# Optimization experiments

Hardware: AMD Instinct MI355X
Metric: run time of the kernel (lower is better)

The kernel has to match this reference:

```python
import jax, jax.numpy as jnp
import numpy as np

N_NODES = 100000
N_EDGES = 3200000
IN_DIM = 256


def gcn_conv(x, src, dst, W, b):
    # PyG GCNConv: add self-loops, symmetric normalization D^-1/2 A D^-1/2
    n = x.shape[0]
    loop = jnp.arange(n)
    s = jnp.concatenate([src, loop])
    d = jnp.concatenate([dst, loop])
    deg = jax.ops.segment_sum(jnp.ones(d.shape, x.dtype), d, num_segments=n)
    dinv = jnp.where(deg > 0, jax.lax.rsqrt(deg), 0.0).astype(x.dtype)
    norm = dinv[s] * dinv[d]                      # [E+N]
    h = x @ W                                     # [N, out] transform first (out < in)
    msg = h[s] * norm[:, None]                    # gather + scale
    out = jax.ops.segment_sum(msg, d, num_segments=n)  # scatter-add
    return out + b


def setup_inputs() -> dict:
    key = jax.random.key(0)
    ks = jax.random.split(key, 8)
    x = jax.random.normal(ks[0], (N_NODES, IN_DIM), dtype=jnp.float32)
    edge_index = jax.random.randint(ks[1], (2, N_EDGES), 0, N_NODES, dtype=jnp.int64)
    # Glorot-ish scaled params
    W1 = jax.random.normal(ks[2], (IN_DIM, 64), dtype=jnp.float32) / np.sqrt(IN_DIM)
    b1 = jnp.zeros((64,), jnp.float32)
    W2 = jax.random.normal(ks[3], (64, 32), dtype=jnp.float32) / np.sqrt(64)
    b2 = jnp.zeros((32,), jnp.float32)
    fc_w = jax.random.normal(ks[4], (1, 32), dtype=jnp.float32) / np.sqrt(32)
    fc_b = jnp.zeros((1,), jnp.float32)
    return {"x": x, "edge_index": edge_index, "W1": W1, "b1": b1,
            "W2": W2, "b2": b2, "fc_w": fc_w, "fc_b": fc_b}


def reference(x, edge_index, W1, b1, W2, b2, fc_w, fc_b):
    src, dst = edge_index[0], edge_index[1]
    h = jax.nn.relu(gcn_conv(x, src, dst, W1, b1))   # [N, 64]
    h = jax.nn.relu(gcn_conv(h, src, dst, W2, b2))   # [N, 32]
    pooled = h.mean(axis=0)                          # [32]
    return pooled @ fc_w.T + fc_b                    # [1]
```

## Files before the change

kernel.cpp:

```cpp
#include <hip/hip_runtime.h>
#include <hip/hip_fp16.h>

#ifndef F1
#define F1 64
#define F2 32
#endif

#define NBLK 512
#define BSH  7
#define BNODES 128

typedef _Float16 half8 __attribute__((ext_vector_type(8)));
typedef float floatx4 __attribute__((ext_vector_type(4)));

__global__ __launch_bounds__(256) void scan_blocks_kernel(const int* __restrict__ in,
                                                          int* __restrict__ tmp,
                                                          int* __restrict__ blk_sums, int n) {
    __shared__ int sdata[256];
    int t = threadIdx.x;
    int base = blockIdx.x * 1024 + t * 4;
    int v[4];
#pragma unroll
    for (int j = 0; j < 4; ++j) v[j] = (base + j < n) ? in[base + j] : 0;
    int mysum = v[0] + v[1] + v[2] + v[3];
    sdata[t] = mysum;
    __syncthreads();
    for (int ofs = 1; ofs < 256; ofs <<= 1) {
        int val = (t >= ofs) ? sdata[t - ofs] : 0;
        __syncthreads();
        sdata[t] += val;
        __syncthreads();
    }
    int incl = sdata[t];
    int excl = incl - mysum;
    if (t == 255) blk_sums[blockIdx.x] = incl;
    int run = excl;
#pragma unroll
    for (int j = 0; j < 4; ++j) {
        if (base + j < n) tmp[base + j] = run;
        run += v[j];
    }
}

__global__ __launch_bounds__(512) void scan_sums_kernel(const int* __restrict__ blk_sums,
                                                        int* __restrict__ blk_scanned, int nb) {
    __shared__ int sdata[512];
    int t = threadIdx.x;
    int mine = (t < nb) ? blk_sums[t] : 0;
    sdata[t] = mine;
    __syncthreads();
    for (int ofs = 1; ofs < 512; ofs <<= 1) {
        int val = (t >= ofs) ? sdata[t - ofs] : 0;
        __syncthreads();
        sdata[t] += val;
        __syncthreads();
    }
    blk_scanned[t] = sdata[t] - mine;
}


__global__ __launch_bounds__(256) void bucket_hist_prep_kernel(const int* __restrict__ dst,
                                                               int* __restrict__ hist_T,
                                                               const float* __restrict__ W1,
                                                               const float* __restrict__ W2,
                                                               __half* __restrict__ W1t,
                                                               __half* __restrict__ W2t,
                                                               float* __restrict__ out,
                                                               int E, int CH, int NB) {
    int b = blockIdx.x;
    if (b == NBLK) {
        if (threadIdx.x == 0) out[0] = 0.f;
        for (int e = threadIdx.x; e < 64 * 256; e += 256) {
            int n = e >> 8, k = e & 255;
            W1t[e] = __float2half(W1[k * 64 + n]);
        }
        for (int e = threadIdx.x; e < 32 * 64; e += 256) {
            int n = e >> 6, k = e & 63;
            W2t[e] = __float2half(W2[k * 32 + n]);
        }
        return;
    }
    __shared__ int lh[1024];
    for (int i = threadIdx.x; i < NB; i += 256) lh[i] = 0;
    __syncthreads();
    int start = b * CH, end = min(E, start + CH);
    for (int e0 = start + threadIdx.x * 4; e0 < end; e0 += 1024) {
        if (e0 + 4 <= end) {
            int4 d4 = *reinterpret_cast<const int4*>(dst + e0);
            atomicAdd(&lh[d4.x >> BSH], 1);
            atomicAdd(&lh[d4.y >> BSH], 1);
            atomicAdd(&lh[d4.z >> BSH], 1);
            atomicAdd(&lh[d4.w >> BSH], 1);
        } else {
            for (int e = e0; e < end; ++e) atomicAdd(&lh[dst[e] >> BSH], 1);
        }
    }
    __syncthreads();
    for (int k = threadIdx.x; k < NB; k += 256)
        hist_T[k * NBLK + b] = lh[k];
}

__global__ __launch_bounds__(256) void bucket_scatter_kernel(const int* __restrict__ src,
                                                             const int* __restrict__ dst,
                                                             const int* __restrict__ tmp,
                                                             const int* __restrict__ bscan,
                                                             int* __restrict__ buck,
                                                             int E, int CH, int NB) {
    __shared__ int cur[1024];
    int b = blockIdx.x;
    for (int i = threadIdx.x; i < NB; i += 256) {
        int idx = i * NBLK + b;
        cur[i] = tmp[idx] + bscan[idx >> 10];
    }
    __syncthreads();
    int start = b * CH, end = min(E, start + CH);
    for (int e0 = start + threadIdx.x * 4; e0 < end; e0 += 1024) {
        if (e0 + 4 <= end) {
            int4 s4 = *reinterpret_cast<const int4*>(src + e0);
            int4 d4 = *reinterpret_cast<const int4*>(dst + e0);
            int p0 = atomicAdd(&cur[d4.x >> BSH], 1);
            buck[p0] = (s4.x << BSH) | (d4.x & (BNODES - 1));
            int p1 = atomicAdd(&cur[d4.y >> BSH], 1);
            buck[p1] = (s4.y << BSH) | (d4.y & (BNODES - 1));
            int p2 = atomicAdd(&cur[d4.z >> BSH], 1);
            buck[p2] = (s4.z << BSH) | (d4.z & (BNODES - 1));
            int p3 = atomicAdd(&cur[d4.w >> BSH], 1);
            buck[p3] = (s4.w << BSH) | (d4.w & (BNODES - 1));
        } else {
            for (int e = e0; e < end; ++e) {
                int d = dst[e];
                int pos = atomicAdd(&cur[d >> BSH], 1);
                buck[pos] = (src[e] << BSH) | (d & (BNODES - 1));
            }
        }
    }
}

__global__ __launch_bounds__(256) void bucket_deg_fill_kernel(const int* __restrict__ buck,
                                                              const int* __restrict__ tmp,
                                                              const int* __restrict__ bscan,
                                                              int* __restrict__ deg,
                                                              float* __restrict__ dinv,
                                                              int* __restrict__ row_off,
                                                              int* __restrict__ csr,
                                                              int E, int N, int NB) {
    __shared__ int cnt[BNODES];
    __shared__ int sc[BNODES];
    __shared__ int lrow[BNODES];
    __shared__ int lcur[BNODES];
    int k = blockIdx.x;
    int tid = threadIdx.x;
    if (tid < BNODES) { cnt[tid] = 0; lcur[tid] = 0; }
    __syncthreads();
    int i0 = k * NBLK;
    int bs = tmp[i0] + bscan[i0 >> 10];
    int be = E;
    if (k + 1 < NB) {
        int i1 = (k + 1) * NBLK;
        be = tmp[i1] + bscan[i1 >> 10];
    }
    for (int e = bs + tid; e < be; e += 256)
        atomicAdd(&cnt[buck[e] & (BNODES - 1)], 1);
    __syncthreads();
    if (tid < BNODES) sc[tid] = cnt[tid];
    __syncthreads();
    for (int ofs = 1; ofs < BNODES; ofs <<= 1) {
        int v = (tid >= ofs && tid < BNODES) ? sc[tid - ofs] : 0;
        __syncthreads();
        if (tid < BNODES) sc[tid] += v;
        __syncthreads();
    }
    if (tid < BNODES) {
        int excl = sc[tid] - cnt[tid];
        lrow[tid] = bs + excl;
        int i = (k << BSH) + tid;
        if (i < N) {
            deg[i] = cnt[tid];
            dinv[i] = rsqrtf((float)(cnt[tid] + 1));
            row_off[i] = bs + excl;
        }
    }
    __syncthreads();
    for (int e = bs + tid; e < be; e += 256) {
        int p = buck[e];
        int li = p & (BNODES - 1);
        int pos = lrow[li] + atomicAdd(&lcur[li], 1);
        csr[pos] = p >> BSH;
    }
}


__device__ __forceinline__ int swz(int p, int r) { return (p ^ ((r >> 1) & 3)) << 4; }

template <bool AF32, int K, int BN>
__global__ __launch_bounds__(256) void gemm_mfma_kernel(const void* __restrict__ Aptr,
                                                        const __half* __restrict__ Bt,
                                                        const float* __restrict__ dinv,
                                                        __half* __restrict__ C,
                                                        int M) {
    constexpr int NT = BN / 16;
    __shared__ half8 Ash[64 * 4];
    __shared__ half8 Bsh[BN * 4];
    char* Ab = (char*)Ash;
    char* Bb = (char*)Bsh;
    int tid = threadIdx.x;
    int w = tid >> 6;
    int l = tid & 63;
    int row0 = blockIdx.x * 64;
    int sr = tid >> 2, sp = tid & 3;
    int fr = l & 15, fp = l >> 4;
    int arow = w * 16 + fr;
    int a_off = arow * 64 + swz(fp, arow);

    floatx4 acc[NT];
#pragma unroll
    for (int c = 0; c < NT; ++c) acc[c] = (floatx4){0.f, 0.f, 0.f, 0.f};

    for (int k0 = 0; k0 < K; k0 += 32) {
        half8 av = {};
        int gr = row0 + sr;
        if (gr < M) {
            if constexpr (AF32) {
                const float* A = (const float*)Aptr;
                float4 f0 = *(const float4*)(A + (size_t)gr * K + k0 + sp * 8);
                float4 f1 = *(const float4*)(A + (size_t)gr * K + k0 + sp * 8 + 4);
                av[0] = (_Float16)f0.x; av[1] = (_Float16)f0.y;
                av[2] = (_Float16)f0.z; av[3] = (_Float16)f0.w;
                av[4] = (_Float16)f1.x; av[5] = (_Float16)f1.y;
                av[6] = (_Float16)f1.z; av[7] = (_Float16)f1.w;
            } else {
                const __half* A = (const __half*)Aptr;
                av = *(const half8*)(A + (size_t)gr * K + k0 + sp * 8);
            }
        }
        *(half8*)(Ab + sr * 64 + swz(sp, sr)) = av;
        if (tid < BN * 4) {
            int n = tid >> 2, p = tid & 3;
            half8 bv = *(const half8*)(Bt + (size_t)n * K + k0 + p * 8);
            *(half8*)(Bb + n * 64 + swz(p, n)) = bv;
        }
        __syncthreads();
        half8 a = *(const half8*)(Ab + a_off);
#pragma unroll
        for (int c = 0; c < NT; ++c) {
            int col = c * 16 + fr;
            half8 b = *(const half8*)(Bb + col * 64 + swz(fp, col));
            acc[c] = __builtin_amdgcn_mfma_f32_16x16x32_f16(a, b, acc[c], 0, 0, 0);
        }
        __syncthreads();
    }
#pragma unroll
    for (int i = 0; i < 4; ++i) {
        int r = row0 + w * 16 + fp * 4 + i;
        if (r < M) {
            float dn = dinv[r];
#pragma unroll
            for (int c = 0; c < NT; ++c)
                C[(size_t)r * BN + c * 16 + fr] = __float2half(acc[c][i] * dn);
        }
    }
}


__device__ __forceinline__ void acc_row16(const __half* __restrict__ base, float* a) {
    uint4 raw = *reinterpret_cast<const uint4*>(base);
    float2 f0 = __half22float2(*reinterpret_cast<const __half2*>(&raw.x));
    float2 f1 = __half22float2(*reinterpret_cast<const __half2*>(&raw.y));
    float2 f2 = __half22float2(*reinterpret_cast<const __half2*>(&raw.z));
    float2 f3 = __half22float2(*reinterpret_cast<const __half2*>(&raw.w));
    a[0] += f0.x; a[1] += f0.y; a[2] += f1.x; a[3] += f1.y;
    a[4] += f2.x; a[5] += f2.y; a[6] += f3.x; a[7] += f3.y;
}

__device__ __forceinline__ void acc_pk_raw(uint4 raw, __half2* c2) {
    c2[0] = __hadd2(c2[0], *reinterpret_cast<const __half2*>(&raw.x));
    c2[1] = __hadd2(c2[1], *reinterpret_cast<const __half2*>(&raw.y));
    c2[2] = __hadd2(c2[2], *reinterpret_cast<const __half2*>(&raw.z));
    c2[3] = __hadd2(c2[3], *reinterpret_cast<const __half2*>(&raw.w));
}

__device__ __forceinline__ void flush_pk(__half2* c2, float* a) {
#pragma unroll
    for (int j = 0; j < 4; ++j) {
        float2 f = __half22float2(c2[j]);
        a[2 * j] += f.x;
        a[2 * j + 1] += f.y;
        c2[j] = __float2half2_rn(0.f);
    }
}


__global__ __launch_bounds__(256) void agg1_kernel(const __half* __restrict__ g1,
                                                   const int* __restrict__ row_off,
                                                   const int* __restrict__ deg,
                                                   const int* __restrict__ csr,
                                                   const float* __restrict__ dinv,
                                                   const float* __restrict__ b1,
                                                   __half* __restrict__ h1, int n) {
    int node = (blockIdx.x * 256 + threadIdx.x) >> 6;
    int lane = threadIdx.x & 63;
    int g = lane >> 3;
    int f8 = lane & 7;
    if (node >= n) return;
    int start = row_off[node];
    int end = start + deg[node];
    float a[8];
#pragma unroll
    for (int j = 0; j < 8; ++j) a[j] = 0.f;
    if (g == 0)
        acc_row16(g1 + ((size_t)node << 6) + f8 * 8, a);
    __half2 c2[4];
#pragma unroll
    for (int j = 0; j < 4; ++j) c2[j] = __float2half2_rn(0.f);
    int e = start;
    for (; e + 32 <= end; e += 32) {
        int i0 = csr[e + g];
        int i1 = csr[e + 8 + g];
        int i2 = csr[e + 16 + g];
        int i3 = csr[e + 24 + g];
        uint4 r0 = *reinterpret_cast<const uint4*>(g1 + ((size_t)i0 << 6) + f8 * 8);
        uint4 r1 = *reinterpret_cast<const uint4*>(g1 + ((size_t)i1 << 6) + f8 * 8);
        uint4 r2 = *reinterpret_cast<const uint4*>(g1 + ((size_t)i2 << 6) + f8 * 8);
        uint4 r3 = *reinterpret_cast<const uint4*>(g1 + ((size_t)i3 << 6) + f8 * 8);
        acc_pk_raw(r0, c2);
        acc_pk_raw(r1, c2);
        acc_pk_raw(r2, c2);
        acc_pk_raw(r3, c2);
        flush_pk(c2, a);
    }
    if (e + 16 <= end) {
        int i0 = csr[e + g];
        int i1 = csr[e + 8 + g];
        uint4 r0 = *reinterpret_cast<const uint4*>(g1 + ((size_t)i0 << 6) + f8 * 8);
        uint4 r1 = *reinterpret_cast<const uint4*>(g1 + ((size_t)i1 << 6) + f8 * 8);
        acc_pk_raw(r0, c2);
        acc_pk_raw(r1, c2);
        e += 16;
    }
    if (e + 8 <= end) {
        int s = csr[e + g];
        uint4 r = *reinterpret_cast<const uint4*>(g1 + ((size_t)s << 6) + f8 * 8);
        acc_pk_raw(r, c2);
        e += 8;
    }
    if (e + g < end) {
        int s = csr[e + g];
        uint4 r = *reinterpret_cast<const uint4*>(g1 + ((size_t)s << 6) + f8 * 8);
        acc_pk_raw(r, c2);
    }
    flush_pk(c2, a);
#pragma unroll
    for (int j = 0; j < 8; ++j) a[j] += __shfl_xor(a[j], 8);
#pragma unroll
    for (int j = 0; j < 8; ++j) a[j] += __shfl_xor(a[j], 16);
#pragma unroll
    for (int j = 0; j < 8; ++j) a[j] += __shfl_xor(a[j], 32);
    if (g == 0) {
        float dn = dinv[node];
        float4 bl = *reinterpret_cast<const float4*>(b1 + f8 * 8);
        float4 bh = *reinterpret_cast<const float4*>(b1 + f8 * 8 + 4);
        __half hh[8];
        hh[0] = __float2half(fmaxf(a[0] * dn + bl.x, 0.f));
        hh[1] = __float2half(fmaxf(a[1] * dn + bl.y, 0.f));
        hh[2] = __float2half(fmaxf(a[2] * dn + bl.z, 0.f));
        hh[3] = __float2half(fmaxf(a[3] * dn + bl.w, 0.f));
        hh[4] = __float2half(fmaxf(a[4] * dn + bh.x, 0.f));
        hh[5] = __float2half(fmaxf(a[5] * dn + bh.y, 0.f));
        hh[6] = __float2half(fmaxf(a[6] * dn + bh.z, 0.f));
        hh[7] = __float2half(fmaxf(a[7] * dn + bh.w, 0.f));
        *reinterpret_cast<uint4*>(h1 + ((size_t)node << 6) + f8 * 8) =
            *reinterpret_cast<const uint4*>(hh);
    }
}


__global__ __launch_bounds__(256) void agg2_pool_kernel(const __half* __restrict__ g2,
                                                        const int* __restrict__ row_off,
                                                        const int* __restrict__ deg,
                                                        const int* __restrict__ csr,
                                                        const float* __restrict__ dinv,
                                                        const float* __restrict__ b2,
                                                        float* __restrict__ partials,
                                                        int nblocks, int n) {
    int tid = threadIdx.x;
    int half = tid >> 5;
    int node = blockIdx.x * 8 + half;
    int l32 = tid & 31;
    int g = (l32 >> 2);
    int f4 = l32 & 3;
    float a[8];
#pragma unroll
    for (int j = 0; j < 8; ++j) a[j] = 0.f;
    if (node < n) {
        int start = row_off[node];
        int end = start + deg[node];
        if (g == 0)
            acc_row16(g2 + ((size_t)node << 5) + f4 * 8, a);
        __half2 c2[4];
#pragma unroll
        for (int j = 0; j < 4; ++j) c2[j] = __float2half2_rn(0.f);
        int e = start;
        for (; e + 32 <= end; e += 32) {
            int i0 = csr[e + g];
            int i1 = csr[e + 8 + g];
            int i2 = csr[e + 16 + g];
            int i3 = csr[e + 24 + g];
            uint4 r0 = *reinterpret_cast<const uint4*>(g2 + ((size_t)i0 << 5) + f4 * 8);
            uint4 r1 = *reinterpret_cast<const uint4*>(g2 + ((size_t)i1 << 5) + f4 * 8);
            uint4 r2 = *reinterpret_cast<const uint4*>(g2 + ((size_t)i2 << 5) + f4 * 8);
            uint4 r3 = *reinterpret_cast<const uint4*>(g2 + ((size_t)i3 << 5) + f4 * 8);
            acc_pk_raw(r0, c2);
            acc_pk_raw(r1, c2);
            acc_pk_raw(r2, c2);
            acc_pk_raw(r3, c2);
            flush_pk(c2, a);
        }
        if (e + 16 <= end) {
            int i0 = csr[e + g];
            int i1 = csr[e + 8 + g];
            uint4 r0 = *reinterpret_cast<const uint4*>(g2 + ((size_t)i0 << 5) + f4 * 8);
            uint4 r1 = *reinterpret_cast<const uint4*>(g2 + ((size_t)i1 << 5) + f4 * 8);
            acc_pk_raw(r0, c2);
            acc_pk_raw(r1, c2);
            e += 16;
        }
        if (e + 8 <= end) {
            int s = csr[e + g];
            uint4 r = *reinterpret_cast<const uint4*>(g2 + ((size_t)s << 5) + f4 * 8);
            acc_pk_raw(r, c2);
            e += 8;
        }
        if (e + g < end) {
            int s = csr[e + g];
            uint4 r = *reinterpret_cast<const uint4*>(g2 + ((size_t)s << 5) + f4 * 8);
            acc_pk_raw(r, c2);
        }
        flush_pk(c2, a);
#pragma unroll
        for (int j = 0; j < 8; ++j) a[j] += __shfl_xor(a[j], 4);
#pragma unroll
        for (int j = 0; j < 8; ++j) a[j] += __shfl_xor(a[j], 8);
#pragma unroll
        for (int j = 0; j < 8; ++j) a[j] += __shfl_xor(a[j], 16);
    }
    __shared__ float sdata[8][32];
    if (g == 0) {
        float relu[8];
        if (node < n) {
            float dn = dinv[node];
#pragma unroll
            for (int j = 0; j < 8; ++j)
                relu[j] = fmaxf(a[j] * dn + b2[f4 * 8 + j], 0.f);
        } else {
#pragma unroll
            for (int j = 0; j < 8; ++j) relu[j] = 0.f;
        }
#pragma unroll
        for (int j = 0; j < 8; ++j) sdata[half][f4 * 8 + j] = relu[j];
    }
    __syncthreads();
    if (tid < 32) {
        float s = 0.f;
#pragma unroll
        for (int r = 0; r < 8; ++r) s += sdata[r][tid];
        partials[tid * nblocks + blockIdx.x] = s;
    }
}

__global__ __launch_bounds__(256) void reduce_fc_kernel(const float* __restrict__ partials,
                                                        int nblocks,
                                                        const float* __restrict__ fcw,
                                                        const float* __restrict__ fcb,
                                                        float* __restrict__ out, int n) {
    int f = blockIdx.x;
    const float* col = partials + (size_t)f * nblocks;
    float s = 0.f;
    for (int i = threadIdx.x; i < nblocks; i += 256) s += col[i];
    __shared__ float red[256];
    red[threadIdx.x] = s;
    __syncthreads();
    for (int ofs = 128; ofs > 0; ofs >>= 1) {
        if (threadIdx.x < ofs) red[threadIdx.x] += red[threadIdx.x + ofs];
        __syncthreads();
    }
    if (threadIdx.x == 0) {
        float v = (float)((double)red[0] / (double)n * (double)fcw[f]);
        if (f == 0) v += fcb[0];
        atomicAdd(out, v);
    }
}


extern "C" void kernel_launch(void* const* d_in, const int* in_sizes, int n_in,
                              void* d_out, int out_size, void* d_ws, size_t ws_size,
                              hipStream_t stream) {
    const float* x   = (const float*)d_in[0];
    const int*   ei  = (const int*)d_in[1];
    const float* W1  = (const float*)d_in[2];
    const float* b1  = (const float*)d_in[3];
    const float* W2  = (const float*)d_in[4];
    const float* b2  = (const float*)d_in[5];
    const float* fcw = (const float*)d_in[6];
    const float* fcb = (const float*)d_in[7];
    float* out = (float*)d_out;

    const int N = in_sizes[0] / 256;
    const int E = in_sizes[1] / 2;
    const int* src = ei;
    const int* dst = ei + E;

    const int NB = (N + BNODES - 1) >> BSH;
    const int SC = NB * NBLK;
    const int CH = (((E + NBLK - 1) / NBLK) + 3) & ~3;
    const int nb2 = (N + 7) / 8;

    char* ws = (char*)d_ws;
    size_t off = 0;
    auto alloc = [&](size_t bytes) -> void* {
        void* p = ws + off;
        off = (off + bytes + 255) & ~(size_t)255;
        return p;
    };
    int*   tmp      = (int*)alloc((size_t)SC * 4);
    int*   bsums    = (int*)alloc(2048);
    int*   bscan    = (int*)alloc(2048);
    int*   row_off  = (int*)alloc((size_t)N * 4);
    int*   deg      = (int*)alloc((size_t)N * 4);
    float* dinv     = (float*)alloc((size_t)N * 4);
    int*   csr      = (int*)alloc((size_t)E * 4);
    __half* W1t     = (__half*)alloc((size_t)64 * 256 * 2);
    __half* W2t     = (__half*)alloc((size_t)32 * 64 * 2);
    size_t szP = (size_t)E * 4;
    size_t szG1 = (size_t)N * F1 * 2;
    void* P = alloc(szP > szG1 ? szP : szG1);
    int*    buck = (int*)P;
    __half* g1   = (__half*)P;
    int*   hist_T   = (int*)alloc((size_t)SC * 4);
    __half* h1      = (__half*)alloc((size_t)N * F1 * 2);
    __half* g2      = (__half*)alloc((size_t)N * F2 * 2);
    float* partials = (float*)alloc((size_t)F2 * nb2 * 4);

    bucket_hist_prep_kernel<<<NBLK + 1, 256, 0, stream>>>(dst, hist_T, W1, W2, W1t, W2t, out, E, CH, NB);
    int nbS = (SC + 1023) / 1024;
    scan_blocks_kernel<<<nbS, 256, 0, stream>>>(hist_T, tmp, bsums, SC);
    scan_sums_kernel<<<1, 512, 0, stream>>>(bsums, bscan, nbS);
    bucket_scatter_kernel<<<NBLK, 256, 0, stream>>>(src, dst, tmp, bscan, buck, E, CH, NB);
    bucket_deg_fill_kernel<<<NB, 256, 0, stream>>>(buck, tmp, bscan, deg, dinv, row_off, csr, E, N, NB);

    int nbG = (N + 63) / 64;
    gemm_mfma_kernel<true, 256, 64><<<nbG, 256, 0, stream>>>(x, W1t, dinv, g1, N);
    agg1_kernel<<<(N + 3) / 4, 256, 0, stream>>>(g1, row_off, deg, csr, dinv, b1, h1, N);

    gemm_mfma_kernel<false, 64, 32><<<nbG, 256, 0, stream>>>(h1, W2t, dinv, g2, N);
    agg2_pool_kernel<<<nb2, 256, 0, stream>>>(g2, row_off, deg, csr, dinv, b2, partials, nb2, N);

    reduce_fc_kernel<<<F2, 256, 0, stream>>>(partials, nb2, fcw, fcb, out, N);
}
```

Baseline: 211.3 us.

## Fuse CSR build stages into a single cooperative kernel with grid syncs

After: 482.2 us. +128.1%, slower.

```diff
diff --git a/kernel.cpp b/kernel.cpp
--- a/kernel.cpp
+++ b/kernel.cpp
@@ -1,5 +1,8 @@
 #include <hip/hip_runtime.h>
 #include <hip/hip_fp16.h>
+#include <hip/hip_cooperative_groups.h>
+
+namespace cg = cooperative_groups;
 
 #ifndef F1
 #define F1 64
@@ -13,179 +16,180 @@
 typedef _Float16 half8 __attribute__((ext_vector_type(8)));
 typedef float floatx4 __attribute__((ext_vector_type(4)));
 
-__global__ __launch_bounds__(256) void scan_blocks_kernel(const int* __restrict__ in,
-                                                          int* __restrict__ tmp,
-                                                          int* __restrict__ blk_sums, int n) {
-    __shared__ int sdata[256];
-    int t = threadIdx.x;
-    int base = blockIdx.x * 1024 + t * 4;
-    int v[4];
-#pragma unroll
-    for (int j = 0; j < 4; ++j) v[j] = (base + j < n) ? in[base + j] : 0;
-    int mysum = v[0] + v[1] + v[2] + v[3];
-    sdata[t] = mysum;
-    __syncthreads();
-    for (int ofs = 1; ofs < 256; ofs <<= 1) {
-        int val = (t >= ofs) ? sdata[t - ofs] : 0;
-        __syncthreads();
-        sdata[t] += val;
-        __syncthreads();
-    }
-    int incl = sdata[t];
-    int excl = incl - mysum;
-    if (t == 255) blk_sums[blockIdx.x] = incl;
-    int run = excl;
-#pragma unroll
-    for (int j = 0; j < 4; ++j) {
-        if (base + j < n) tmp[base + j] = run;
-        run += v[j];
-    }
-}
-
-__global__ __launch_bounds__(512) void scan_sums_kernel(const int* __restrict__ blk_sums,
-                                                        int* __restrict__ blk_scanned, int nb) {
-    __shared__ int sdata[512];
-    int t = threadIdx.x;
-    int mine = (t < nb) ? blk_sums[t] : 0;
-    sdata[t] = mine;
-    __syncthreads();
-    for (int ofs = 1; ofs < 512; ofs <<= 1) {
-        int val = (t >= ofs) ? sdata[t - ofs] : 0;
-        __syncthreads();
-        sdata[t] += val;
-        __syncthreads();
-    }
-    blk_scanned[t] = sdata[t] - mine;
-}
-
-
-__global__ __launch_bounds__(256) void bucket_hist_prep_kernel(const int* __restrict__ dst,
-                                                               int* __restrict__ hist_T,
-                                                               const float* __restrict__ W1,
-                                                               const float* __restrict__ W2,
-                                                               __half* __restrict__ W1t,
-                                                               __half* __restrict__ W2t,
-                                                               float* __restrict__ out,
-                                                               int E, int CH, int NB) {
-    int b = blockIdx.x;
-    if (b == NBLK) {
-        if (threadIdx.x == 0) out[0] = 0.f;
-        for (int e = threadIdx.x; e < 64 * 256; e += 256) {
-            int n = e >> 8, k = e & 255;
-            W1t[e] = __float2half(W1[k * 64 + n]);
-        }
-        for (int e = threadIdx.x; e < 32 * 64; e += 256) {
-            int n = e >> 6, k = e & 63;
-            W2t[e] = __float2half(W2[k * 32 + n]);
-        }
-        return;
-    }
+
+__global__ __launch_bounds__(256) void csr_build_coop(const int* __restrict__ src,
+                                                      const int* __restrict__ dst,
+                                                      int* __restrict__ hist_T,
+                                                      int* __restrict__ tmp,
+                                                      int* __restrict__ bsums,
+                                                      int* __restrict__ bscan,
+                                                      int* __restrict__ buck,
+                                                      int* __restrict__ deg,
+                                                      float* __restrict__ dinv,
+                                                      int* __restrict__ row_off,
+                                                      int* __restrict__ csr,
+                                                      const float* __restrict__ W1,
+                                                      const float* __restrict__ W2,
+                                                      __half* __restrict__ W1t,
+                                                      __half* __restrict__ W2t,
+                                                      float* __restrict__ out,
+                                                      int E, int CH, int NB, int N, int nbS) {
+    cg::grid_group grid = cg::this_grid();
     __shared__ int lh[1024];
-    for (int i = threadIdx.x; i < NB; i += 256) lh[i] = 0;
-    __syncthreads();
-    int start = b * CH, end = min(E, start + CH);
-    for (int e0 = start + threadIdx.x * 4; e0 < end; e0 += 1024) {
-        if (e0 + 4 <= end) {
-            int4 d4 = *reinterpret_cast<const int4*>(dst + e0);
-            atomicAdd(&lh[d4.x >> BSH], 1);
-            atomicAdd(&lh[d4.y >> BSH], 1);
-            atomicAdd(&lh[d4.z >> BSH], 1);
-            atomicAdd(&lh[d4.w >> BSH], 1);
-        } else {
-            for (int e = e0; e < end; ++e) atomicAdd(&lh[dst[e] >> BSH], 1);
-        }
-    }
-    __syncthreads();
-    for (int k = threadIdx.x; k < NB; k += 256)
-        hist_T[k * NBLK + b] = lh[k];
-}
-
-__global__ __launch_bounds__(256) void bucket_scatter_kernel(const int* __restrict__ src,
-                                                             const int* __restrict__ dst,
-                                                             const int* __restrict__ tmp,
-                                                             const int* __restrict__ bscan,
-                                                             int* __restrict__ buck,
-                                                             int E, int CH, int NB) {
-    __shared__ int cur[1024];
-    int b = blockIdx.x;
-    for (int i = threadIdx.x; i < NB; i += 256) {
-        int idx = i * NBLK + b;
-        cur[i] = tmp[idx] + bscan[idx >> 10];
-    }
-    __syncthreads();
-    int start = b * CH, end = min(E, start + CH);
-    for (int e0 = start + threadIdx.x * 4; e0 < end; e0 += 1024) {
-        if (e0 + 4 <= end) {
-            int4 s4 = *reinterpret_cast<const int4*>(src + e0);
-            int4 d4 = *reinterpret_cast<const int4*>(dst + e0);
-            int p0 = atomicAdd(&cur[d4.x >> BSH], 1);
-            buck[p0] = (s4.x << BSH) | (d4.x & (BNODES - 1));
-            int p1 = atomicAdd(&cur[d4.y >> BSH], 1);
-            buck[p1] = (s4.y << BSH) | (d4.y & (BNODES - 1));
-            int p2 = atomicAdd(&cur[d4.z >> BSH], 1);
-            buck[p2] = (s4.z << BSH) | (d4.z & (BNODES - 1));
-            int p3 = atomicAdd(&cur[d4.w >> BSH], 1);
-            buck[p3] = (s4.w << BSH) | (d4.w & (BNODES - 1));
-        } else {
-            for (int e = e0; e < end; ++e) {
-                int d = dst[e];
-                int pos = atomicAdd(&cur[d >> BSH], 1);
-                buck[pos] = (src[e] << BSH) | (d & (BNODES - 1));
-            }
-        }
-    }
-}
-
-__global__ __launch_bounds__(256) void bucket_deg_fill_kernel(const int* __restrict__ buck,
-                                                              const int* __restrict__ tmp,
-                                                              const int* __restrict__ bscan,
-                                                              int* __restrict__ deg,
-                                                              float* __restrict__ dinv,
-                                                              int* __restrict__ row_off,
-                                                              int* __restrict__ csr,
-                                                              int E, int N, int NB) {
     __shared__ int cnt[BNODES];
     __shared__ int sc[BNODES];
     __shared__ int lrow[BNODES];
     __shared__ int lcur[BNODES];
-    int k = blockIdx.x;
+    int b = blockIdx.x;
     int tid = threadIdx.x;
-    if (tid < BNODES) { cnt[tid] = 0; lcur[tid] = 0; }
-    __syncthreads();
-    int i0 = k * NBLK;
-    int bs = tmp[i0] + bscan[i0 >> 10];
-    int be = E;
-    if (k + 1 < NB) {
-        int i1 = (k + 1) * NBLK;
-        be = tmp[i1] + bscan[i1 >> 10];
-    }
-    for (int e = bs + tid; e < be; e += 256)
-        atomicAdd(&cnt[buck[e] & (BNODES - 1)], 1);
-    __syncthreads();
-    if (tid < BNODES) sc[tid] = cnt[tid];
-    __syncthreads();
-    for (int ofs = 1; ofs < BNODES; ofs <<= 1) {
-        int v = (tid >= ofs && tid < BNODES) ? sc[tid - ofs] : 0;
-        __syncthreads();
-        if (tid < BNODES) sc[tid] += v;
-        __syncthreads();
-    }
-    if (tid < BNODES) {
-        int excl = sc[tid] - cnt[tid];
-        lrow[tid] = bs + excl;
-        int i = (k << BSH) + tid;
-        if (i < N) {
-            deg[i] = cnt[tid];
-            dinv[i] = rsqrtf((float)(cnt[tid] + 1));
-            row_off[i] = bs + excl;
-        }
-    }
-    __syncthreads();
-    for (int e = bs + tid; e < be; e += 256) {
-        int p = buck[e];
-        int li = p & (BNODES - 1);
-        int pos = lrow[li] + atomicAdd(&lcur[li], 1);
-        csr[pos] = p >> BSH;
+    int SC = NB * NBLK;
+
+    if (b == NBLK) {
+        if (tid == 0) out[0] = 0.f;
+        for (int e = tid; e < 64 * 256; e += 256) {
+            int n = e >> 8, k = e & 255;
+            W1t[e] = __float2half(W1[k * 64 + n]);
+        }
+        for (int e = tid; e < 32 * 64; e += 256) {
+            int n = e >> 6, k = e & 63;
+            W2t[e] = __float2half(W2[k * 32 + n]);
+        }
+    } else {
+        for (int i = tid; i < NB; i += 256) lh[i] = 0;
+        __syncthreads();
+        int start = b * CH, end = min(E, start + CH);
+        for (int e0 = start + tid * 4; e0 < end; e0 += 1024) {
+            if (e0 + 4 <= end) {
+                int4 d4 = *reinterpret_cast<const int4*>(dst + e0);
+                atomicAdd(&lh[d4.x >> BSH], 1);
+                atomicAdd(&lh[d4.y >> BSH], 1);
+                atomicAdd(&lh[d4.z >> BSH], 1);
+                atomicAdd(&lh[d4.w >> BSH], 1);
+            } else {
+                for (int e = e0; e < end; ++e) atomicAdd(&lh[dst[e] >> BSH], 1);
+            }
+        }
+        __syncthreads();
+        for (int k = tid; k < NB; k += 256)
+            hist_T[k * NBLK + b] = lh[k];
+    }
+    grid.sync();
+
+    if (b < nbS) {
+        int base = b * 1024 + tid * 4;
+        int v[4];
+#pragma unroll
+        for (int j = 0; j < 4; ++j) v[j] = (base + j < SC) ? hist_T[base + j] : 0;
+        int mysum = v[0] + v[1] + v[2] + v[3];
+        lh[tid] = mysum;
+        __syncthreads();
+        for (int ofs = 1; ofs < 256; ofs <<= 1) {
+            int val = (tid >= ofs) ? lh[tid - ofs] : 0;
+            __syncthreads();
+            lh[tid] += val;
+            __syncthreads();
+        }
+        int incl = lh[tid];
+        int excl = incl - mysum;
+        if (tid == 255) bsums[b] = incl;
+        int run = excl;
+#pragma unroll
+        for (int j = 0; j < 4; ++j) {
+            if (base + j < SC) tmp[base + j] = run;
+            run += v[j];
+        }
+    }
+    grid.sync();
+
+    if (b == 0) {
+        int i0 = 2 * tid, i1 = 2 * tid + 1;
+        int v0 = (i0 < nbS) ? bsums[i0] : 0;
+        int v1 = (i1 < nbS) ? bsums[i1] : 0;
+        lh[i0] = v0;
+        lh[i1] = v1;
+        __syncthreads();
+        for (int ofs = 1; ofs < 512; ofs <<= 1) {
+            int a0 = (i0 >= ofs) ? lh[i0 - ofs] : 0;
+            int a1 = (i1 >= ofs) ? lh[i1 - ofs] : 0;
+            __syncthreads();
+            lh[i0] += a0;
+            lh[i1] += a1;
+            __syncthreads();
+        }
+        bscan[i0] = lh[i0] - v0;
+        bscan[i1] = lh[i1] - v1;
+    }
+    grid.sync();
+
+    if (b < NBLK) {
+        for (int i = tid; i < NB; i += 256) {
+            int idx = i * NBLK + b;
+            lh[i] = tmp[idx] + bscan[idx >> 10];
+        }
+        __syncthreads();
+        int start = b * CH, end = min(E, start + CH);
+        for (int e0 = start + tid * 4; e0 < end; e0 += 1024) {
+            if (e0 + 4 <= end) {
+                int4 s4 = *reinterpret_cast<const int4*>(src + e0);
+                int4 d4 = *reinterpret_cast<const int4*>(dst + e0);
+                int p0 = atomicAdd(&lh[d4.x >> BSH], 1);
+                buck[p0] = (s4.x << BSH) | (d4.x & (BNODES - 1));
+                int p1 = atomicAdd(&lh[d4.y >> BSH], 1);
+                buck[p1] = (s4.y << BSH) | (d4.y & (BNODES - 1));
+                int p2 = atomicAdd(&lh[d4.z >> BSH], 1);
+                buck[p2] = (s4.z << BSH) | (d4.z & (BNODES - 1));
+                int p3 = atomicAdd(&lh[d4.w >> BSH], 1);
+                buck[p3] = (s4.w << BSH) | (d4.w & (BNODES - 1));
+            } else {
+                for (int e = e0; e < end; ++e) {
+                    int d = dst[e];
+                    int pos = atomicAdd(&lh[d >> BSH], 1);
+                    buck[pos] = (src[e] << BSH) | (d & (BNODES - 1));
+                }
+            }
+        }
+    }
+    grid.sync();
+
+    for (int k = b; k < NB; k += gridDim.x) {
+        if (tid < BNODES) { cnt[tid] = 0; lcur[tid] = 0; }
+        __syncthreads();
+        int i0 = k * NBLK;
+        int bs = tmp[i0] + bscan[i0 >> 10];
+        int be = E;
+        if (k + 1 < NB) {
+            int i1 = (k + 1) * NBLK;
+            be = tmp[i1] + bscan[i1 >> 10];
+        }
+        for (int e = bs + tid; e < be; e += 256)
+            atomicAdd(&cnt[buck[e] & (BNODES - 1)], 1);
+        __syncthreads();
+        if (tid < BNODES) sc[tid] = cnt[tid];
+        __syncthreads();
+        for (int ofs = 1; ofs < BNODES; ofs <<= 1) {
+            int v = (tid >= ofs && tid < BNODES) ? sc[tid - ofs] : 0;
+            __syncthreads();
+            if (tid < BNODES) sc[tid] += v;
+            __syncthreads();
+        }
+        if (tid < BNODES) {
+            int excl = sc[tid] - cnt[tid];
+            lrow[tid] = bs + excl;
+            int i = (k << BSH) + tid;
+            if (i < N) {
+                deg[i] = cnt[tid];
+                dinv[i] = rsqrtf((float)(cnt[tid] + 1));
+                row_off[i] = bs + excl;
+            }
+        }
+        __syncthreads();
+        for (int e = bs + tid; e < be; e += 256) {
+            int p = buck[e];
+            int li = p & (BNODES - 1);
+            int pos = lrow[li] + atomicAdd(&lcur[li], 1);
+            csr[pos] = p >> BSH;
+        }
+        __syncthreads();
     }
 }
 
@@ -505,14 +509,15 @@
     float* out = (float*)d_out;
 
     const int N = in_sizes[0] / 256;
-    const int E = in_sizes[1] / 2;
+    int E = in_sizes[1] / 2;
     const int* src = ei;
     const int* dst = ei + E;
 
-    const int NB = (N + BNODES - 1) >> BSH;
+    int NB = (N + BNODES - 1) >> BSH;
     const int SC = NB * NBLK;
-    const int CH = (((E + NBLK - 1) / NBLK) + 3) & ~3;
+    int CH = (((E + NBLK - 1) / NBLK) + 3) & ~3;
     const int nb2 = (N + 7) / 8;
+    int nbS = (SC + 1023) / 1024;
 
     char* ws = (char*)d_ws;
     size_t off = 0;
@@ -540,12 +545,11 @@
     __half* g2      = (__half*)alloc((size_t)N * F2 * 2);
     float* partials = (float*)alloc((size_t)F2 * nb2 * 4);
 
-    bucket_hist_prep_kernel<<<NBLK + 1, 256, 0, stream>>>(dst, hist_T, W1, W2, W1t, W2t, out, E, CH, NB);
-    int nbS = (SC + 1023) / 1024;
-    scan_blocks_kernel<<<nbS, 256, 0, stream>>>(hist_T, tmp, bsums, SC);
-    scan_sums_kernel<<<1, 512, 0, stream>>>(bsums, bscan, nbS);
-    bucket_scatter_kernel<<<NBLK, 256, 0, stream>>>(src, dst, tmp, bscan, buck, E, CH, NB);
-    bucket_deg_fill_kernel<<<NB, 256, 0, stream>>>(buck, tmp, bscan, deg, dinv, row_off, csr, E, N, NB);
+    void* args[] = {&src, &dst, &hist_T, &tmp, &bsums, &bscan, &buck, &deg, &dinv,
+                    &row_off, &csr, &W1, &W2, &W1t, &W2t, &out,
+                    &E, &CH, &NB, (void*)&N, &nbS};
+    hipLaunchCooperativeKernel((void*)csr_build_coop, dim3(NBLK + 1), dim3(256),
+                               args, 0, stream);
 
     int nbG = (N + 63) / 64;
     gemm_mfma_kernel<true, 256, 64><<<nbG, 256, 0, stream>>>(x, W1t, dinv, g1, N);
```

## Locally sort edges per block in shared memory before bucket scatter

Applied to the files above, without the earlier changes.

Result: faster. 196.9 us (-6.8%).

```diff
diff --git a/kernel.cpp b/kernel.cpp
--- a/kernel.cpp
+++ b/kernel.cpp
@@ -9,6 +9,7 @@
 #define NBLK 512
 #define BSH  7
 #define BNODES 128
+#define CHMAX 6272
 
 typedef _Float16 half8 __attribute__((ext_vector_type(8)));
 typedef float floatx4 __attribute__((ext_vector_type(4)));
@@ -81,7 +82,7 @@
         return;
     }
     __shared__ int lh[1024];
-    for (int i = threadIdx.x; i < NB; i += 256) lh[i] = 0;
+    for (int i = threadIdx.x; i < 1024; i += 256) lh[i] = 0;
     __syncthreads();
     int start = b * CH, end = min(E, start + CH);
     for (int e0 = start + threadIdx.x * 4; e0 < end; e0 += 1024) {
@@ -100,39 +101,83 @@
         hist_T[k * NBLK + b] = lh[k];
 }
 
-__global__ __launch_bounds__(256) void bucket_scatter_kernel(const int* __restrict__ src,
+
+__global__ __launch_bounds__(256) void scatter_sorted_kernel(const int* __restrict__ src,
                                                              const int* __restrict__ dst,
                                                              const int* __restrict__ tmp,
                                                              const int* __restrict__ bscan,
                                                              int* __restrict__ buck,
                                                              int E, int CH, int NB) {
-    __shared__ int cur[1024];
+    __shared__ int hoff[1024];
+    __shared__ int lhist[1024];
+    __shared__ int sc[1024];
+    __shared__ int lcur[1024];
+    __shared__ int sorted[CHMAX];
+    __shared__ unsigned short sbkt[CHMAX];
     int b = blockIdx.x;
-    for (int i = threadIdx.x; i < NB; i += 256) {
+    int tid = threadIdx.x;
+    for (int i = tid; i < 1024; i += 256) lhist[i] = 0;
+    for (int i = tid; i < NB; i += 256) {
         int idx = i * NBLK + b;
-        cur[i] = tmp[idx] + bscan[idx >> 10];
+        hoff[i] = tmp[idx] + bscan[idx >> 10];
     }
     __syncthreads();
     int start = b * CH, end = min(E, start + CH);
-    for (int e0 = start + threadIdx.x * 4; e0 < end; e0 += 1024) {
+    int count = end - start;
+    for (int e0 = start + tid * 4; e0 < end; e0 += 1024) {
+        if (e0 + 4 <= end) {
+            int4 d4 = *reinterpret_cast<const int4*>(dst + e0);
+            atomicAdd(&lhist[d4.x >> BSH], 1);
+            atomicAdd(&lhist[d4.y >> BSH], 1);
+            atomicAdd(&lhist[d4.z >> BSH], 1);
+            atomicAdd(&lhist[d4.w >> BSH], 1);
+        } else {
+            for (int e = e0; e < end; ++e) atomicAdd(&lhist[dst[e] >> BSH], 1);
+        }
+    }
+    __syncthreads();
+    for (int i = tid; i < 1024; i += 256) sc[i] = lhist[i];
+    __syncthreads();
+    for (int ofs = 1; ofs < 1024; ofs <<= 1) {
+        int i1 = tid + 256, i2 = tid + 512, i3 = tid + 768;
+        int v0 = (tid >= ofs) ? sc[tid - ofs] : 0;
+        int v1 = (i1 >= ofs) ? sc[i1 - ofs] : 0;
+        int v2 = (i2 >= ofs) ? sc[i2 - ofs] : 0;
+        int v3 = (i3 >= ofs) ? sc[i3 - ofs] : 0;
+        __syncthreads();
+        sc[tid] += v0; sc[i1] += v1; sc[i2] += v2; sc[i3] += v3;
+        __syncthreads();
+    }
+    for (int i = tid; i < 1024; i += 256) {
+        int ex = sc[i] - lhist[i];
+        sc[i] = ex;
+        lcur[i] = ex;
+    }
+    __syncthreads();
+    for (int e0 = start + tid * 4; e0 < end; e0 += 1024) {
         if (e0 + 4 <= end) {
             int4 s4 = *reinterpret_cast<const int4*>(src + e0);
             int4 d4 = *reinterpret_cast<const int4*>(dst + e0);
-            int p0 = atomicAdd(&cur[d4.x >> BSH], 1);
-            buck[p0] = (s4.x << BSH) | (d4.x & (BNODES - 1));
-            int p1 = atomicAdd(&cur[d4.y >> BSH], 1);
-            buck[p1] = (s4.y << BSH) | (d4.y & (BNODES - 1));
-            int p2 = atomicAdd(&cur[d4.z >> BSH], 1);
-            buck[p2] = (s4.z << BSH) | (d4.z & (BNODES - 1));
-            int p3 = atomicAdd(&cur[d4.w >> BSH], 1);
-            buck[p3] = (s4.w << BSH) | (d4.w & (BNODES - 1));
+            int k0 = d4.x >> BSH, p0 = atomicAdd(&lcur[k0], 1);
+            sorted[p0] = (s4.x << BSH) | (d4.x & (BNODES - 1)); sbkt[p0] = (unsigned short)k0;
+            int k1 = d4.y >> BSH, p1 = atomicAdd(&lcur[k1], 1);
+            sorted[p1] = (s4.y << BSH) | (d4.y & (BNODES - 1)); sbkt[p1] = (unsigned short)k1;
+            int k2 = d4.z >> BSH, p2 = atomicAdd(&lcur[k2], 1);
+            sorted[p2] = (s4.z << BSH) | (d4.z & (BNODES - 1)); sbkt[p2] = (unsigned short)k2;
+            int k3 = d4.w >> BSH, p3 = atomicAdd(&lcur[k3], 1);
+            sorted[p3] = (s4.w << BSH) | (d4.w & (BNODES - 1)); sbkt[p3] = (unsigned short)k3;
         } else {
             for (int e = e0; e < end; ++e) {
                 int d = dst[e];
-                int pos = atomicAdd(&cur[d >> BSH], 1);
-                buck[pos] = (src[e] << BSH) | (d & (BNODES - 1));
+                int k = d >> BSH, p = atomicAdd(&lcur[k], 1);
+                sorted[p] = (src[e] << BSH) | (d & (BNODES - 1)); sbkt[p] = (unsigned short)k;
             }
         }
+    }
+    __syncthreads();
+    for (int p = tid; p < count; p += 256) {
+        int k = sbkt[p];
+        buck[hoff[k] + (p - sc[k])] = sorted[p];
     }
 }
 
@@ -544,7 +589,7 @@
     int nbS = (SC + 1023) / 1024;
     scan_blocks_kernel<<<nbS, 256, 0, stream>>>(hist_T, tmp, bsums, SC);
     scan_sums_kernel<<<1, 512, 0, stream>>>(bsums, bscan, nbS);
-    bucket_scatter_kernel<<<NBLK, 256, 0, stream>>>(src, dst, tmp, bscan, buck, E, CH, NB);
+    scatter_sorted_kernel<<<NBLK, 256, 0, stream>>>(src, dst, tmp, bscan, buck, E, CH, NB);
     bucket_deg_fill_kernel<<<NB, 256, 0, stream>>>(buck, tmp, bscan, deg, dinv, row_off, csr, E, N, NB);
 
     int nbG = (N + 63) / 64;
```
